# Kernel optimization log

Hardware: AMD Instinct MI355X
Metric: run time of the kernel (lower is better)

The kernel has to match this reference:

```python
import jax, jax.numpy as jnp
import numpy as np

B, H, S, D, T = 2, 32, 8192, 128, 512


def setup_inputs() -> dict:
    key = jax.random.key(0)
    k1, k2, k3, k4 = jax.random.split(key, 4)
    return {
        "cache_k": jax.random.normal(k1, (B, H, S, D), dtype=jnp.float32),
        "cache_v": jax.random.normal(k2, (B, H, S, D), dtype=jnp.float32),
        "new_k": jax.random.normal(k3, (B, H, T, D), dtype=jnp.float32),
        "new_v": jax.random.normal(k4, (B, H, T, D), dtype=jnp.float32),
        "position_ids": jnp.arange(T, dtype=jnp.int64),  # contiguous prefill positions
    }


def reference(cache_k, cache_v, new_k, new_v, position_ids):
    # torch: cache.scatter(2, pos.expand(B,H,T,D), new) with unique positions
    # == write new_k/new_v rows into the cache along the sequence axis.
    updated_k = cache_k.at[:, :, position_ids, :].set(new_k)
    updated_v = cache_v.at[:, :, position_ids, :].set(new_v)
    return (updated_k, updated_v)
```

## Files before the change

### kernel.cpp

```cpp
#include <hip/hip_runtime.h>


#define S_LEN 8192
#define T_LEN 512
#define D_DIM 128
#define BH    64
#define ELEMS_PER_TENSOR (BH * S_LEN * D_DIM)
#define VECS_PER_BH      (S_LEN * (D_DIM / 4))
#define NEW_VECS_PER_BH  (T_LEN * (D_DIM / 4))

typedef float f4_t __attribute__((ext_vector_type(4)));

__global__ __launch_bounds__(256) void ssc_fused(
    const f4_t* __restrict__ ck, const f4_t* __restrict__ cv,
    const f4_t* __restrict__ nk, const f4_t* __restrict__ nv,
    const void* __restrict__ pos,
    f4_t* __restrict__ ok, f4_t* __restrict__ ov) {

    __shared__ int lmap[8];
    const int ltid = threadIdx.x;
    const int s0   = blockIdx.x * 8;

    if (ltid < 8) lmap[ltid] = -1;
    __syncthreads();

    {
        const long long* p64 = (const long long*)pos;
        const int*       p32 = (const int*)pos;
        long long a = p64[0], b = p64[1];
        bool is64 = (a >= 0) && (a < S_LEN) && (b >= 0) && (b < S_LEN) && (a != b);
        #pragma unroll
        for (int j = ltid; j < T_LEN; j += 256) {
            int p = is64 ? (int)p64[j] : p32[j];
            unsigned r = (unsigned)(p - s0);
            if (r < 8u) lmap[r] = j;
        }
    }
    __syncthreads();

    const int tid = blockIdx.x * 256 + ltid;
    const int d4  = tid & 31;
    const int s   = tid >> 5;
    const int t   = lmap[s & 7];

    const f4_t* csrc = blockIdx.z ? cv : ck;
    const f4_t* nsrc = blockIdx.z ? nv : nk;
    f4_t*       odst = blockIdx.z ? ov : ok;

    const int bh0    = blockIdx.y * (BH / 2);
    const int dstOff = s * 32 + d4;

    const f4_t* src;
    int sstride;
    if (t >= 0) { src = nsrc + (t * 32 + d4) + bh0 * NEW_VECS_PER_BH; sstride = NEW_VECS_PER_BH; }
    else        { src = csrc + dstOff          + bh0 * VECS_PER_BH;    sstride = VECS_PER_BH; }
    f4_t* dst = odst + dstOff + bh0 * VECS_PER_BH;

    #pragma unroll 4
    for (int i = 0; i < BH / 2; ++i) {
        f4_t v = __builtin_nontemporal_load(src);
        __builtin_nontemporal_store(v, dst);
        src += sstride;
        dst += VECS_PER_BH;
    }
}

extern "C" void kernel_launch(void* const* d_in, const int* in_sizes, int n_in,
                              void* d_out, int out_size, void* d_ws, size_t ws_size,
                              hipStream_t stream) {
    const f4_t* ck = (const f4_t*)d_in[0];
    const f4_t* cv = (const f4_t*)d_in[1];
    const f4_t* nk = (const f4_t*)d_in[2];
    const f4_t* nv = (const f4_t*)d_in[3];
    const void* pos = d_in[4];

    float* out = (float*)d_out;
    f4_t* ok = (f4_t*)out;
    f4_t* ov = (f4_t*)(out + ELEMS_PER_TENSOR);

    ssc_fused<<<dim3(1024, 2, 2), 256, 0, stream>>>(ck, cv, nk, nv, pos, ok, ov);
}
```

Measured before the change: 197.3 us.

## Remap blocks to contiguous 256-row chunks per head instead of strided heads

Each block now covers 256 consecutive sequence rows of a single batch-head, looping over 32 row groups with a 256-entry shared position map. The old layout had each thread stride across 32 batch-heads. The new layout gives each block a contiguous 128KB span, which should improve DRAM page locality and cut the per-block position-map work relative to the data moved. Stores are now regular stores rather than nontemporal, and the per-row lmap lookup adds shared-memory reads and a branch per iteration.

```diff
diff --git a/kernel.cpp b/kernel.cpp
--- a/kernel.cpp
+++ b/kernel.cpp
@@ -17,11 +17,12 @@
     const void* __restrict__ pos,
     f4_t* __restrict__ ok, f4_t* __restrict__ ov) {
 
-    __shared__ int lmap[8];
+    __shared__ int lmap[256];
     const int ltid = threadIdx.x;
-    const int s0   = blockIdx.x * 8;
+    const int bh   = blockIdx.y * (BH / 2) + (blockIdx.x >> 5);
+    const int s0   = (blockIdx.x & 31) * 256;
 
-    if (ltid < 8) lmap[ltid] = -1;
+    lmap[ltid] = -1;
     __syncthreads();
 
     {
@@ -33,35 +34,28 @@
         for (int j = ltid; j < T_LEN; j += 256) {
             int p = is64 ? (int)p64[j] : p32[j];
             unsigned r = (unsigned)(p - s0);
-            if (r < 8u) lmap[r] = j;
+            if (r < 256u) lmap[r] = j;
         }
     }
     __syncthreads();
-
-    const int tid = blockIdx.x * 256 + ltid;
-    const int d4  = tid & 31;
-    const int s   = tid >> 5;
-    const int t   = lmap[s & 7];
 
     const f4_t* csrc = blockIdx.z ? cv : ck;
     const f4_t* nsrc = blockIdx.z ? nv : nk;
     f4_t*       odst = blockIdx.z ? ov : ok;
 
-    const int bh0    = blockIdx.y * (BH / 2);
-    const int dstOff = s * 32 + d4;
+    const int chunkBase = bh * VECS_PER_BH + s0 * 32;
+    const f4_t* cbase = csrc + chunkBase + ltid;
+    f4_t*       dbase = odst + chunkBase + ltid;
+    const f4_t* nbase = nsrc + bh * NEW_VECS_PER_BH + (ltid & 31);
+    const int   rlane = ltid >> 5;
 
-    const f4_t* src;
-    int sstride;
-    if (t >= 0) { src = nsrc + (t * 32 + d4) + bh0 * NEW_VECS_PER_BH; sstride = NEW_VECS_PER_BH; }
-    else        { src = csrc + dstOff          + bh0 * VECS_PER_BH;    sstride = VECS_PER_BH; }
-    f4_t* dst = odst + dstOff + bh0 * VECS_PER_BH;
-
-    #pragma unroll 4
-    for (int i = 0; i < BH / 2; ++i) {
-        f4_t v = __builtin_nontemporal_load(src);
-        __builtin_nontemporal_store(v, dst);
-        src += sstride;
-        dst += VECS_PER_BH;
+    #pragma unroll 8
+    for (int i = 0; i < 32; ++i) {
+        const int t = lmap[i * 8 + rlane];
+        f4_t v;
+        if (t >= 0) v = nbase[t * 32];
+        else        v = __builtin_nontemporal_load(cbase + i * 256);
+        dbase[i * 256] = v;
     }
 }
 
```

New measurement: 209.0 us. 5.9% more time.
